# Kernel optimization log

Hardware: AMD Instinct MI355X
Metric: run time of the kernel (lower is better)

The kernel has to match this reference:

```python
import jax, jax.numpy as jnp
import numpy as np

B, N, D, K = 32, 8192, 256, 16
NUM_ITERS = 3
QUALITY_THRESHOLD = 0.3
W_ATTN, W_LEARNED, W_CONF = 0.4, 0.4, 0.2


def _ln(x, g, b, eps=1e-5):
    m = jnp.mean(x, axis=-1, keepdims=True)
    v = jnp.mean((x - m) ** 2, axis=-1, keepdims=True)
    return (x - m) * jax.lax.rsqrt(v + eps) * g + b


def setup_inputs() -> dict:
    key = jax.random.key(0)
    ks = jax.random.split(key, 24)
    s = 0.02
    inp = {
        'inputs': jax.random.normal(ks[0], (B, N, D), dtype=jnp.float32),
        'semantic_confidence': jax.random.uniform(ks[1], (B, K), dtype=jnp.float32),
        'slot_inits': jax.random.normal(ks[2], (K, D), dtype=jnp.float32) * 0.02,
        'ln_in_g': jnp.ones((D,), jnp.float32),
        'ln_in_b': jnp.zeros((D,), jnp.float32),
        'Wq': jax.random.normal(ks[3], (D, D), jnp.float32) * s,
        'Wk': jax.random.normal(ks[4], (D, D), jnp.float32) * s,
        'Wv': jax.random.normal(ks[5], (D, D), jnp.float32) * s,
        'gru_wih': jax.random.normal(ks[6], (3 * D, D), jnp.float32) * s,
        'gru_whh': jax.random.normal(ks[7], (3 * D, D), jnp.float32) * s,
        'gru_bih': jnp.zeros((3 * D,), jnp.float32),
        'gru_bhh': jnp.zeros((3 * D,), jnp.float32),
        'mlp_ln_g': jnp.ones((D,), jnp.float32),
        'mlp_ln_b': jnp.zeros((D,), jnp.float32),
        'mlp_w1': jax.random.normal(ks[8], (2 * D, D), jnp.float32) * s,
        'mlp_b1': jnp.zeros((2 * D,), jnp.float32),
        'mlp_w2': jax.random.normal(ks[9], (D, 2 * D), jnp.float32) * s,
        'mlp_b2': jnp.zeros((D,), jnp.float32),
        'sel_w1': jax.random.normal(ks[10], (D // 2, D), jnp.float32) * s,
        'sel_b1': jnp.zeros((D // 2,), jnp.float32),
        'sel_w2': jax.random.normal(ks[11], (1, D // 2), jnp.float32) * s,
        'sel_b2': jnp.zeros((1,), jnp.float32),
        'qn_w1': jax.random.normal(ks[12], (D // 4, D), jnp.float32) * s,
        'qn_b1': jnp.zeros((D // 4,), jnp.float32),
        'qn_w2': jax.random.normal(ks[13], (1, D // 4), jnp.float32) * s,
        'qn_b2': jnp.zeros((1,), jnp.float32),
    }
    return inp


def _forward(inputs, semantic_confidence, slot_inits, ln_in_g, ln_in_b, Wq, Wk, Wv,
             gru_wih, gru_whh, gru_bih, gru_bhh, mlp_ln_g, mlp_ln_b,
             mlp_w1, mlp_b1, mlp_w2, mlp_b2, sel_w1, sel_b1, sel_w2, sel_b2,
             qn_w1, qn_b1, qn_w2, qn_b2):
    b, n, d = inputs.shape
    kk = slot_inits.shape[0]
    scale = d ** -0.5
    x = _ln(inputs, ln_in_g, ln_in_b)                     # [B,N,D]
    k = x @ Wk.T                                          # [B,N,D] (constant across iters)
    v = x @ Wv.T                                          # [B,N,D]
    slots = jnp.broadcast_to(slot_inits[None], (b, kk, d))
    attn = None
    for _ in range(NUM_ITERS):
        q = slots @ Wq.T                                  # [B,K,D]
        logits = jnp.einsum('bkd,bnd->bkn', q, k) * scale
        attn = jax.nn.softmax(logits, axis=1)             # competition over slots
        updates = jnp.einsum('bkn,bnd->bkd', attn, v)
        # GRUCell: h' = (1-z)*n_g + z*h
        gi = updates @ gru_wih.T + gru_bih                # [B,K,3D]
        gh = slots @ gru_whh.T + gru_bhh
        i_r, i_z, i_n = jnp.split(gi, 3, axis=-1)
        h_r, h_z, h_n = jnp.split(gh, 3, axis=-1)
        r = jax.nn.sigmoid(i_r + h_r)
        z = jax.nn.sigmoid(i_z + h_z)
        n_g = jnp.tanh(i_n + r * h_n)
        slots = (1.0 - z) * n_g + z * slots
        # residual MLP
        h = _ln(slots, mlp_ln_g, mlp_ln_b)
        h = jax.nn.relu(h @ mlp_w1.T + mlp_b1) @ mlp_w2.T + mlp_b2
        slots = slots + h
    final_attn = attn                                     # [B,K,N]
    winners = jnp.argmax(final_attn, axis=1)              # [B,N]
    onehot = (winners[:, None, :] == jnp.arange(kk)[None, :, None]).astype(final_attn.dtype)
    winning_attn = jnp.sum(final_attn * onehot, axis=-1)  # [B,K]
    total_attn = jnp.sum(final_attn, axis=-1)
    attn_quality = winning_attn / (total_attn + 1e-8)
    # learned quality
    lq = jax.nn.relu(slots @ qn_w1.T + qn_b1)
    learned_quality = jax.nn.sigmoid((lq @ qn_w2.T + qn_b2)[..., 0])  # [B,K]
    quality = W_ATTN * attn_quality + W_LEARNED * learned_quality
    quality = quality * W_CONF + semantic_confidence * (1.0 - W_CONF)
    # adaptive selection (eval path: sigmoid threshold)
    sh = jax.nn.relu(slots @ sel_w1.T + sel_b1)
    sel_logits = (sh @ sel_w2.T + sel_b2)[..., 0]         # [B,K]
    sel_mask = (jax.nn.sigmoid(sel_logits) > 0.5).astype(slots.dtype)
    sel_mask = sel_mask * (quality > QUALITY_THRESHOLD).astype(slots.dtype)
    attn_weights = jnp.transpose(final_attn, (0, 2, 1))   # [B,N,K]
    return slots, sel_mask, quality, attn_weights


def reference(inputs, semantic_confidence, slot_inits, ln_in_g, ln_in_b, Wq, Wk, Wv,
              gru_wih, gru_whh, gru_bih, gru_bhh, mlp_ln_g, mlp_ln_b,
              mlp_w1, mlp_b1, mlp_w2, mlp_b2, sel_w1, sel_b1, sel_w2, sel_b2,
              qn_w1, qn_b1, qn_w2, qn_b2):
    return _forward(inputs, semantic_confidence, slot_inits, ln_in_g, ln_in_b, Wq, Wk, Wv,
                    gru_wih, gru_whh, gru_bih, gru_bhh, mlp_ln_g, mlp_ln_b,
                    mlp_w1, mlp_b1, mlp_w2, mlp_b2, sel_w1, sel_b1, sel_w2, sel_b2,
                    qn_w1, qn_b1, qn_w2, qn_b2)
```

## Files before the change

### kernel.cpp

```cpp
#include <hip/hip_runtime.h>

#define BB 32
#define NN 8192
#define DD 256
#define KK 16

typedef __bf16  bf16x8 __attribute__((ext_vector_type(8)));
typedef float   f32x4  __attribute__((ext_vector_type(4)));
typedef unsigned short us8 __attribute__((ext_vector_type(8)));

__device__ __forceinline__ unsigned short f2bf(float f) {
  unsigned u = __builtin_bit_cast(unsigned, f);
  u += 0x7fffu + ((u >> 16) & 1u);
  return (unsigned short)(u >> 16);
}
__device__ __forceinline__ float bf2f(unsigned short h) {
  unsigned u = ((unsigned)h) << 16;
  return __builtin_bit_cast(float, u);
}
__device__ __forceinline__ float sigm(float x) { return 1.f / (1.f + __expf(-x)); }
__device__ __forceinline__ float tanh_fast(float x) { return 1.f - 2.f / (__expf(2.f * x) + 1.f); }

__device__ __forceinline__ void gl2lds16(const void* g, void* l) {
  __builtin_amdgcn_global_load_lds((const __attribute__((address_space(1))) unsigned int*)g,
                                   (__attribute__((address_space(3))) unsigned int*)l, 16, 0, 0);
}

__global__ __launch_bounds__(256) void k_init(const float* __restrict__ Wk, const float* __restrict__ Wv,
                                              const float* __restrict__ sinit,
                                              unsigned short* __restrict__ Wkvb, float* __restrict__ slots) {
  int idx = blockIdx.x * 256 + threadIdx.x;
  int row = idx >> 8, col = idx & 255;
  float w = (row < 256) ? Wk[row * 256 + col] : Wv[(row - 256) * 256 + col];
  Wkvb[idx] = f2bf(w);
  slots[idx] = sinit[(row & 15) * 256 + col];
}

__global__ __launch_bounds__(256) void k_proj(const float* __restrict__ X, const float* __restrict__ lng,
                                              const float* __restrict__ lnb,
                                              const unsigned short* __restrict__ Wkvb,
                                              unsigned short* __restrict__ kv) {
  __shared__ __attribute__((aligned(16))) char bt[2][33280];
  const int wave = threadIdx.x >> 6, lane = threadIdx.x & 63;
  const int c16 = lane & 15, quad = lane >> 4;
  const int row0 = blockIdx.x * 256 + wave * 64;

  bf16x8 af[4][8];
#pragma unroll
  for (int s = 0; s < 4; ++s) {
    const int row = row0 + s * 16 + c16;
    const float* xr = X + (long)row * 256;
    float v[8][8];
    float sum = 0.f, sq = 0.f;
#pragma unroll
    for (int fi = 0; fi < 8; ++fi) {
      const float4 a0 = *(const float4*)(xr + fi * 32 + quad * 8);
      const float4 a1 = *(const float4*)(xr + fi * 32 + quad * 8 + 4);
      v[fi][0] = a0.x; v[fi][1] = a0.y; v[fi][2] = a0.z; v[fi][3] = a0.w;
      v[fi][4] = a1.x; v[fi][5] = a1.y; v[fi][6] = a1.z; v[fi][7] = a1.w;
      sum += a0.x + a0.y + a0.z + a0.w + a1.x + a1.y + a1.z + a1.w;
      sq += a0.x * a0.x + a0.y * a0.y + a0.z * a0.z + a0.w * a0.w +
            a1.x * a1.x + a1.y * a1.y + a1.z * a1.z + a1.w * a1.w;
    }
    sum += __shfl_xor(sum, 16); sum += __shfl_xor(sum, 32);
    sq  += __shfl_xor(sq, 16);  sq  += __shfl_xor(sq, 32);
    const float mean = sum * (1.f / 256.f);
    const float rstd = rsqrtf(sq * (1.f / 256.f) - mean * mean + 1e-5f);
#pragma unroll
    for (int fi = 0; fi < 8; ++fi) {
      const int dbase = fi * 32 + quad * 8;
      const float4 g0 = *(const float4*)(lng + dbase), g1 = *(const float4*)(lng + dbase + 4);
      const float4 b0 = *(const float4*)(lnb + dbase), b1 = *(const float4*)(lnb + dbase + 4);
      us8 t;
      t[0] = f2bf((v[fi][0] - mean) * rstd * g0.x + b0.x);
      t[1] = f2bf((v[fi][1] - mean) * rstd * g0.y + b0.y);
      t[2] = f2bf((v[fi][2] - mean) * rstd * g0.z + b0.z);
      t[3] = f2bf((v[fi][3] - mean) * rstd * g0.w + b0.w);
      t[4] = f2bf((v[fi][4] - mean) * rstd * g1.x + b1.x);
      t[5] = f2bf((v[fi][5] - mean) * rstd * g1.y + b1.y);
      t[6] = f2bf((v[fi][6] - mean) * rstd * g1.z + b1.z);
      t[7] = f2bf((v[fi][7] - mean) * rstd * g1.w + b1.w);
      af[s][fi] = __builtin_bit_cast(bf16x8, t);
    }
  }

  {
    const char* gw = (const char*)Wkvb;
#pragma unroll
    for (int i = 0; i < 8; ++i) {
      const int p = wave * 8 + i;
      gl2lds16(gw + p * 1024 + lane * 16, &bt[0][p * 1040]);
    }
  }
#pragma unroll 1
  for (int c = 0; c < 8; ++c) {
    __syncthreads();
    if (c < 7) {
      const char* gw = (const char*)Wkvb + (c + 1) * 32768;
#pragma unroll
      for (int i = 0; i < 8; ++i) {
        const int p = wave * 8 + i;
        gl2lds16(gw + p * 1024 + lane * 16, &bt[(c + 1) & 1][p * 1040]);
      }
    }
    const char* bb = bt[c & 1];
#pragma unroll 1
    for (int ot = 0; ot < 4; ++ot) {
      const int tl = ot * 16 + c16;
      const char* bp = bb + (tl >> 1) * 1040 + (tl & 1) * 512 + quad * 16;
      f32x4 acc[4];
#pragma unroll
      for (int s = 0; s < 4; ++s) { acc[s][0] = 0.f; acc[s][1] = 0.f; acc[s][2] = 0.f; acc[s][3] = 0.f; }
#pragma unroll
      for (int fi = 0; fi < 8; ++fi) {
        const bf16x8 bfrag = *(const bf16x8*)(bp + fi * 64);
#pragma unroll
        for (int s = 0; s < 4; ++s)
          acc[s] = __builtin_amdgcn_mfma_f32_16x16x32_bf16(af[s][fi], bfrag, acc[s], 0, 0, 0);
      }
      const int col = c * 64 + ot * 16 + c16;
#pragma unroll
      for (int s = 0; s < 4; ++s) {
#pragma unroll
        for (int r = 0; r < 4; ++r) {
          kv[(long)(row0 + s * 16 + quad * 4 + r) * 512 + col] = f2bf(acc[s][r]);
        }
      }
    }
  }
}

__global__ __launch_bounds__(256) void k_qproj(const float* __restrict__ slots, const float* __restrict__ Wq,
                                               unsigned short* __restrict__ qb) {
  __shared__ float srow[256];
  const int row = blockIdx.x, t = threadIdx.x;
  srow[t] = slots[row * 256 + t];
  __syncthreads();
  float acc = 0.f;
  const float4* wr = (const float4*)(Wq + t * 256);
#pragma unroll 8
  for (int i = 0; i < 64; ++i) {
    float4 w = wr[i];
    float4 s = *(const float4*)(srow + i * 4);
    acc += w.x * s.x + w.y * s.y + w.z * s.z + w.w * s.w;
  }
  qb[row * 256 + t] = f2bf(acc);
}

__device__ __forceinline__ void stage_chunk64(const char* gk, char* buf, int wave, int lane) {
#pragma unroll
  for (int i = 0; i < 16; ++i) {
    const int p = wave * 16 + i;
    const int tp = p & 31;
    const int vh = (p >> 5) * 512;
    gl2lds16(gk + (2 * tp + (lane >> 5)) * 1024 + vh + (lane & 31) * 16, buf + p * 1040);
  }
}

template <bool FINAL>
__global__ __launch_bounds__(256) void k_attn(const unsigned short* __restrict__ kv,
                                              const unsigned short* __restrict__ qb,
                                              float* __restrict__ updates, float* __restrict__ aw,
                                              float* __restrict__ winning, float* __restrict__ total) {
  __shared__ __attribute__((aligned(16))) char sbuf[2][66560];
  __shared__ float lds_attn[4][16][16];
  const int wave = threadIdx.x >> 6, lane = threadIdx.x & 63;
  const int c16 = lane & 15, quad = lane >> 4;
  const int b = blockIdx.x >> 3, slab = blockIdx.x & 7;

  bf16x8 qa[8];
  const unsigned short* qrow = qb + (b * 16 + c16) * 256 + quad * 8;
#pragma unroll
  for (int fi = 0; fi < 8; ++fi) qa[fi] = *(const bf16x8*)(qrow + fi * 32);

  float acc[16][4];
#pragma unroll
  for (int s = 0; s < 16; ++s) { acc[s][0] = 0.f; acc[s][1] = 0.f; acc[s][2] = 0.f; acc[s][3] = 0.f; }

  const char* gk0 = (const char*)kv + ((long)b * 8192 + (long)slab * 1024) * 1024;

  stage_chunk64(gk0, sbuf[0], wave, lane);

#pragma unroll 1
  for (int ch = 0; ch < 16; ++ch) {
    __syncthreads();
    if (ch < 15) stage_chunk64(gk0 + (ch + 1) * 65536, sbuf[(ch + 1) & 1], wave, lane);
    const char* bb = sbuf[ch & 1];

    const int tl = wave * 16 + c16;
    const char* kp = bb + (tl >> 1) * 1040 + (tl & 1) * 512 + quad * 16;
    f32x4 c = {0.f, 0.f, 0.f, 0.f};
#pragma unroll
    for (int fi = 0; fi < 8; ++fi) {
      const bf16x8 bfrag = *(const bf16x8*)(kp + fi * 64);
      c = __builtin_amdgcn_mfma_f32_16x16x32_bf16(qa[fi], bfrag, c, 0, 0, 0);
    }
    float l[4];
#pragma unroll
    for (int r = 0; r < 4; ++r) l[r] = c[r] * 0.0625f;
    float m = l[0]; int mi = quad * 4;
#pragma unroll
    for (int r = 1; r < 4; ++r) { if (l[r] > m) { m = l[r]; mi = quad * 4 + r; } }
#pragma unroll
    for (int off = 16; off < 64; off <<= 1) {
      float om = __shfl_xor(m, off); int oi = __shfl_xor(mi, off);
      if (om > m || (om == m && oi < mi)) { m = om; mi = oi; }
    }
    float e[4], ssum = 0.f;
#pragma unroll
    for (int r = 0; r < 4; ++r) { e[r] = __expf(l[r] - m); ssum += e[r]; }
    ssum += __shfl_xor(ssum, 16); ssum += __shfl_xor(ssum, 32);
    const float inv = 1.f / ssum;
    float a[4];
#pragma unroll
    for (int r = 0; r < 4; ++r) a[r] = e[r] * inv;

    if (FINAL) {
      const int tg = slab * 1024 + ch * 64 + wave * 16 + c16;
      *(float4*)(aw + (long)(b * 8192 + tg) * 16 + quad * 4) = make_float4(a[0], a[1], a[2], a[3]);
      float ts[4] = {a[0], a[1], a[2], a[3]};
#pragma unroll
      for (int off = 1; off < 16; off <<= 1) {
#pragma unroll
        for (int r = 0; r < 4; ++r) ts[r] += __shfl_xor(ts[r], off);
      }
      if (c16 == 0) {
#pragma unroll
        for (int r = 0; r < 4; ++r) atomicAdd(&total[b * 16 + quad * 4 + r], ts[r]);
      }
      if (quad == 0) atomicAdd(&winning[b * 16 + mi], inv);
    }

    *(float4*)&lds_attn[wave][c16][quad * 4] = make_float4(a[0], a[1], a[2], a[3]);

#pragma unroll 4
    for (int nn = 0; nn < 16; ++nn) {
      const int n = wave * 16 + nn;
      const char* vp = bb + (32 + (n >> 1)) * 1040 + (n & 1) * 512 + lane * 8;
      const ushort4 vv = *(const ushort4*)vp;
      const float v0 = bf2f(vv.x), v1 = bf2f(vv.y), v2 = bf2f(vv.z), v3 = bf2f(vv.w);
      const float4 a0 = *(const float4*)&lds_attn[wave][nn][0];
      const float4 a1 = *(const float4*)&lds_attn[wave][nn][4];
      const float4 a2 = *(const float4*)&lds_attn[wave][nn][8];
      const float4 a3 = *(const float4*)&lds_attn[wave][nn][12];
      const float as[16] = {a0.x, a0.y, a0.z, a0.w, a1.x, a1.y, a1.z, a1.w,
                            a2.x, a2.y, a2.z, a2.w, a3.x, a3.y, a3.z, a3.w};
#pragma unroll
      for (int s = 0; s < 16; ++s) {
        acc[s][0] = fmaf(as[s], v0, acc[s][0]);
        acc[s][1] = fmaf(as[s], v1, acc[s][1]);
        acc[s][2] = fmaf(as[s], v2, acc[s][2]);
        acc[s][3] = fmaf(as[s], v3, acc[s][3]);
      }
    }
  }

  __syncthreads();
  float* part = (float*)sbuf;
#pragma unroll
  for (int s = 0; s < 16; ++s)
    *(float4*)&part[(wave * 16 + s) * 256 + lane * 4] =
        make_float4(acc[s][0], acc[s][1], acc[s][2], acc[s][3]);
  __syncthreads();
  float* ub = updates + b * (KK * DD);
#pragma unroll
  for (int i = 0; i < 16; ++i) {
    const int idx = i * 256 + threadIdx.x;
    atomicAdd(&ub[idx], part[idx] + part[4096 + idx] + part[8192 + idx] + part[12288 + idx]);
  }
}

__global__ __launch_bounds__(256) void k_slotup(const float* __restrict__ updates, float* __restrict__ slots,
                                                const float* __restrict__ wih, const float* __restrict__ whh,
                                                const float* __restrict__ bih, const float* __restrict__ bhh,
                                                const float* __restrict__ mlng, const float* __restrict__ mlnb,
                                                const float* __restrict__ w1, const float* __restrict__ b1,
                                                const float* __restrict__ w2, const float* __restrict__ b2) {
  __shared__ float su[4][256];
  __shared__ float ss[4][256];
  __shared__ float sn[4][256];
  __shared__ float h1s[4][512];
  __shared__ float mv[8];
  const int t = threadIdx.x;
  const int r0 = blockIdx.x * 4;
#pragma unroll
  for (int r = 0; r < 4; ++r) {
    su[r][t] = updates[(r0 + r) * 256 + t];
    ss[r][t] = slots[(r0 + r) * 256 + t];
  }
  __syncthreads();
  float giv[3][4], ghv[3][4];
#pragma unroll 1
  for (int p = 0; p < 3; ++p) {
    const int o = p * 256 + t;
    float ai[4], ah[4];
    const float bi = bih[o], bh = bhh[o];
#pragma unroll
    for (int r = 0; r < 4; ++r) { ai[r] = bi; ah[r] = bh; }
    const float4* wi = (const float4*)(wih + o * 256);
    const float4* wh = (const float4*)(whh + o * 256);
#pragma unroll 4
    for (int i = 0; i < 64; ++i) {
      const float4 a = wi[i], hh = wh[i];
#pragma unroll
      for (int r = 0; r < 4; ++r) {
        const float4 u = *(const float4*)&su[r][i * 4];
        const float4 s = *(const float4*)&ss[r][i * 4];
        ai[r] += a.x * u.x + a.y * u.y + a.z * u.z + a.w * u.w;
        ah[r] += hh.x * s.x + hh.y * s.y + hh.z * s.z + hh.w * s.w;
      }
    }
#pragma unroll
    for (int r = 0; r < 4; ++r) { giv[p][r] = ai[r]; ghv[p][r] = ah[r]; }
  }
#pragma unroll
  for (int r = 0; r < 4; ++r) {
    const float rg = sigm(giv[0][r] + ghv[0][r]);
    const float z = sigm(giv[1][r] + ghv[1][r]);
    const float ng = tanh_fast(giv[2][r] + rg * ghv[2][r]);
    sn[r][t] = (1.f - z) * ng + z * ss[r][t];
  }
  __syncthreads();
  const int wv = t >> 6, ln = t & 63;
  {
    const float4 x = *(const float4*)&sn[wv][ln * 4];
    float s = x.x + x.y + x.z + x.w;
    float q = x.x * x.x + x.y * x.y + x.z * x.z + x.w * x.w;
#pragma unroll
    for (int off = 1; off < 64; off <<= 1) { s += __shfl_xor(s, off); q += __shfl_xor(q, off); }
    if (ln == 0) {
      const float mean = s * (1.f / 256.f);
      mv[wv * 2] = mean;
      mv[wv * 2 + 1] = rsqrtf(q * (1.f / 256.f) - mean * mean + 1e-5f);
    }
  }
  __syncthreads();
  const float gt = mlng[t], btv = mlnb[t];
#pragma unroll
  for (int r = 0; r < 4; ++r) ss[r][t] = (sn[r][t] - mv[r * 2]) * mv[r * 2 + 1] * gt + btv;
  __syncthreads();
#pragma unroll 1
  for (int p = 0; p < 2; ++p) {
    const int o = p * 256 + t;
    float a1v[4];
    const float bb1 = b1[o];
#pragma unroll
    for (int r = 0; r < 4; ++r) a1v[r] = bb1;
    const float4* wr = (const float4*)(w1 + o * 256);
#pragma unroll 4
    for (int i = 0; i < 64; ++i) {
      const float4 w = wr[i];
#pragma unroll
      for (int r = 0; r < 4; ++r) {
        const float4 hv = *(const float4*)&ss[r][i * 4];
        a1v[r] += w.x * hv.x + w.y * hv.y + w.z * hv.z + w.w * hv.w;
      }
    }
#pragma unroll
    for (int r = 0; r < 4; ++r) h1s[r][o] = fmaxf(a1v[r], 0.f);
  }
  __syncthreads();
  float a2[4];
  const float bb2 = b2[t];
#pragma unroll
  for (int r = 0; r < 4; ++r) a2[r] = bb2;
  const float4* w2r = (const float4*)(w2 + t * 512);
#pragma unroll 4
  for (int i = 0; i < 128; ++i) {
    const float4 w = w2r[i];
#pragma unroll
    for (int r = 0; r < 4; ++r) {
      const float4 hv = *(const float4*)&h1s[r][i * 4];
      a2[r] += w.x * hv.x + w.y * hv.y + w.z * hv.z + w.w * hv.w;
    }
  }
#pragma unroll
  for (int r = 0; r < 4; ++r) slots[(r0 + r) * 256 + t] = sn[r][t] + a2[r];
}

__global__ __launch_bounds__(256) void k_final(const float* __restrict__ slots, const float* __restrict__ winning,
                                               const float* __restrict__ total, const float* __restrict__ conf,
                                               const float* __restrict__ sw1, const float* __restrict__ sb1,
                                               const float* __restrict__ sw2, const float* __restrict__ sb2,
                                               const float* __restrict__ qw1, const float* __restrict__ qb1,
                                               const float* __restrict__ qw2, const float* __restrict__ qb2,
                                               float* __restrict__ out_slots, float* __restrict__ out_mask,
                                               float* __restrict__ out_quality) {
  __shared__ float srow[256];
  __shared__ float sh[128];
  __shared__ float lq[64];
  const int row = blockIdx.x, t = threadIdx.x;
  srow[t] = slots[row * 256 + t];
  __syncthreads();
  if (t < 128) {
    float acc = sb1[t];
    const float4* wr = (const float4*)(sw1 + t * 256);
#pragma unroll 8
    for (int i = 0; i < 64; ++i) {
      const float4 w = wr[i];
      const float4 s = *(const float4*)(srow + i * 4);
      acc += w.x * s.x + w.y * s.y + w.z * s.z + w.w * s.w;
    }
    sh[t] = fmaxf(acc, 0.f);
  } else if (t < 192) {
    const int o = t - 128;
    float acc = qb1[o];
    const float4* wr = (const float4*)(qw1 + o * 256);
#pragma unroll 8
    for (int i = 0; i < 64; ++i) {
      const float4 w = wr[i];
      const float4 s = *(const float4*)(srow + i * 4);
      acc += w.x * s.x + w.y * s.y + w.z * s.z + w.w * s.w;
    }
    lq[o] = fmaxf(acc, 0.f);
  }
  __syncthreads();
  if (t < 64) {
    float a = sh[t] * sw2[t] + sh[t + 64] * sw2[t + 64];
    float bq = lq[t] * qw2[t];
#pragma unroll
    for (int off = 1; off < 64; off <<= 1) { a += __shfl_xor(a, off); bq += __shfl_xor(bq, off); }
    if (t == 0) {
      const float sel_logit = a + sb2[0];
      const float learned = sigm(bq + qb2[0]);
      const float attq = winning[row] / (total[row] + 1e-8f);
      float qual = 0.4f * attq + 0.4f * learned;
      qual = qual * 0.2f + conf[row] * 0.8f;
      out_quality[row] = qual;
      out_mask[row] = (sel_logit > 0.f && qual > 0.3f) ? 1.f : 0.f;
    }
  }
  out_slots[row * 256 + t] = srow[t];
}

extern "C" void kernel_launch(void* const* d_in, const int* in_sizes, int n_in,
                              void* d_out, int out_size, void* d_ws, size_t ws_size,
                              hipStream_t stream) {
  const float* X = (const float*)d_in[0];
  const float* conf = (const float*)d_in[1];
  const float* sinit = (const float*)d_in[2];
  const float* lng = (const float*)d_in[3];
  const float* lnb = (const float*)d_in[4];
  const float* Wq = (const float*)d_in[5];
  const float* Wk = (const float*)d_in[6];
  const float* Wv = (const float*)d_in[7];
  const float* wih = (const float*)d_in[8];
  const float* whh = (const float*)d_in[9];
  const float* bih = (const float*)d_in[10];
  const float* bhh = (const float*)d_in[11];
  const float* mlng = (const float*)d_in[12];
  const float* mlnb = (const float*)d_in[13];
  const float* w1 = (const float*)d_in[14];
  const float* b1 = (const float*)d_in[15];
  const float* w2 = (const float*)d_in[16];
  const float* b2 = (const float*)d_in[17];
  const float* sw1 = (const float*)d_in[18];
  const float* sb1 = (const float*)d_in[19];
  const float* sw2 = (const float*)d_in[20];
  const float* sb2 = (const float*)d_in[21];
  const float* qw1 = (const float*)d_in[22];
  const float* qb1 = (const float*)d_in[23];
  const float* qw2 = (const float*)d_in[24];
  const float* qb2 = (const float*)d_in[25];

  char* w = (char*)d_ws;
  unsigned short* kv = (unsigned short*)(w);
  unsigned short* Wkvb = (unsigned short*)(w + 268435456);
  unsigned short* qb = (unsigned short*)(w + 268697600);
  float* slots = (float*)(w + 268959744);
  float* updates = (float*)(w + 269484032);
  float* winning = (float*)(w + 270008320);
  float* total = (float*)(w + 270010368);

  float* out_slots = (float*)d_out;
  float* out_mask = out_slots + 131072;
  float* out_quality = out_mask + 512;
  float* aw = out_quality + 512;

  k_init<<<512, 256, 0, stream>>>(Wk, Wv, sinit, Wkvb, slots);
  k_proj<<<1024, 256, 0, stream>>>(X, lng, lnb, Wkvb, kv);
  for (int it = 0; it < 3; ++it) {
    k_qproj<<<512, 256, 0, stream>>>(slots, Wq, qb);
    hipMemsetAsync(updates, 0, 512 * 256 * 4, stream);
    if (it == 2) {
      hipMemsetAsync(winning, 0, 2048, stream);
      hipMemsetAsync(total, 0, 2048, stream);
      k_attn<true><<<256, 256, 0, stream>>>(kv, qb, updates, aw, winning, total);
    } else {
      k_attn<false><<<256, 256, 0, stream>>>(kv, qb, updates, nullptr, nullptr, nullptr);
    }
    k_slotup<<<128, 256, 0, stream>>>(updates, slots, wih, whh, bih, bhh, mlng, mlnb, w1, b1, w2, b2);
  }
  k_final<<<512, 256, 0, stream>>>(slots, winning, total, conf, sw1, sb1, sw2, sb2,
                                   qw1, qb1, qw2, qb2, out_slots, out_mask, out_quality);
}
```

Baseline: 1.079 ms.

## Double attention grid with half-size chunks and load K/V weights directly in projection

The attention kernel now launches 512 blocks, each covering 512 tokens in 32-token chunks. Pairs of waves redundantly compute the same logits and split the value accumulation between them, which halves LDS use and adds parallelism on a GPU with many CUs. The projection kernel drops its LDS double-buffering of the weight matrix and reads B fragments straight from global memory. It also swaps the MFMA operands so each lane can write four contiguous bf16 outputs as one vector store. The costs are redundant logit and softmax work in half of the attention waves, and more global weight traffic in the projection.

```diff
diff --git a/kernel.cpp b/kernel.cpp
--- a/kernel.cpp
+++ b/kernel.cpp
@@ -40,7 +40,6 @@
                                               const float* __restrict__ lnb,
                                               const unsigned short* __restrict__ Wkvb,
                                               unsigned short* __restrict__ kv) {
-  __shared__ __attribute__((aligned(16))) char bt[2][33280];
   const int wave = threadIdx.x >> 6, lane = threadIdx.x & 63;
   const int c16 = lane & 15, quad = lane >> 4;
   const int row0 = blockIdx.x * 256 + wave * 64;
@@ -84,47 +83,29 @@
     }
   }
 
-  {
-    const char* gw = (const char*)Wkvb;
-#pragma unroll
-    for (int i = 0; i < 8; ++i) {
-      const int p = wave * 8 + i;
-      gl2lds16(gw + p * 1024 + lane * 16, &bt[0][p * 1040]);
-    }
-  }
 #pragma unroll 1
   for (int c = 0; c < 8; ++c) {
-    __syncthreads();
-    if (c < 7) {
-      const char* gw = (const char*)Wkvb + (c + 1) * 32768;
-#pragma unroll
-      for (int i = 0; i < 8; ++i) {
-        const int p = wave * 8 + i;
-        gl2lds16(gw + p * 1024 + lane * 16, &bt[(c + 1) & 1][p * 1040]);
-      }
-    }
-    const char* bb = bt[c & 1];
 #pragma unroll 1
     for (int ot = 0; ot < 4; ++ot) {
-      const int tl = ot * 16 + c16;
-      const char* bp = bb + (tl >> 1) * 1040 + (tl & 1) * 512 + quad * 16;
+      const unsigned short* wrow = Wkvb + (c * 64 + ot * 16 + c16) * 256 + quad * 8;
+      bf16x8 bfrag[8];
+#pragma unroll
+      for (int fi = 0; fi < 8; ++fi) bfrag[fi] = *(const bf16x8*)(wrow + fi * 32);
       f32x4 acc[4];
 #pragma unroll
       for (int s = 0; s < 4; ++s) { acc[s][0] = 0.f; acc[s][1] = 0.f; acc[s][2] = 0.f; acc[s][3] = 0.f; }
 #pragma unroll
       for (int fi = 0; fi < 8; ++fi) {
-        const bf16x8 bfrag = *(const bf16x8*)(bp + fi * 64);
 #pragma unroll
         for (int s = 0; s < 4; ++s)
-          acc[s] = __builtin_amdgcn_mfma_f32_16x16x32_bf16(af[s][fi], bfrag, acc[s], 0, 0, 0);
-      }
-      const int col = c * 64 + ot * 16 + c16;
+          acc[s] = __builtin_amdgcn_mfma_f32_16x16x32_bf16(bfrag[fi], af[s][fi], acc[s], 0, 0, 0);
+      }
+      const int colb = c * 64 + ot * 16 + quad * 4;
 #pragma unroll
       for (int s = 0; s < 4; ++s) {
-#pragma unroll
-        for (int r = 0; r < 4; ++r) {
-          kv[(long)(row0 + s * 16 + quad * 4 + r) * 512 + col] = f2bf(acc[s][r]);
-        }
+        ushort4 o;
+        o.x = f2bf(acc[s][0]); o.y = f2bf(acc[s][1]); o.z = f2bf(acc[s][2]); o.w = f2bf(acc[s][3]);
+        *(ushort4*)(kv + (long)(row0 + s * 16 + c16) * 512 + colb) = o;
       }
     }
   }
@@ -147,12 +128,12 @@
   qb[row * 256 + t] = f2bf(acc);
 }
 
-__device__ __forceinline__ void stage_chunk64(const char* gk, char* buf, int wave, int lane) {
-#pragma unroll
-  for (int i = 0; i < 16; ++i) {
-    const int p = wave * 16 + i;
-    const int tp = p & 31;
-    const int vh = (p >> 5) * 512;
+__device__ __forceinline__ void stage_chunk32(const char* gk, char* buf, int wave, int lane) {
+#pragma unroll
+  for (int i = 0; i < 8; ++i) {
+    const int p = wave * 8 + i;
+    const int tp = p & 15;
+    const int vh = (p >> 4) * 512;
     gl2lds16(gk + (2 * tp + (lane >> 5)) * 1024 + vh + (lane & 31) * 16, buf + p * 1040);
   }
 }
@@ -162,11 +143,11 @@
                                               const unsigned short* __restrict__ qb,
                                               float* __restrict__ updates, float* __restrict__ aw,
                                               float* __restrict__ winning, float* __restrict__ total) {
-  __shared__ __attribute__((aligned(16))) char sbuf[2][66560];
+  __shared__ __attribute__((aligned(16))) char sbuf[2][33280];
   __shared__ float lds_attn[4][16][16];
   const int wave = threadIdx.x >> 6, lane = threadIdx.x & 63;
   const int c16 = lane & 15, quad = lane >> 4;
-  const int b = blockIdx.x >> 3, slab = blockIdx.x & 7;
+  const int b = blockIdx.x >> 4, slab = blockIdx.x & 15;
 
   bf16x8 qa[8];
   const unsigned short* qrow = qb + (b * 16 + c16) * 256 + quad * 8;
@@ -177,18 +158,18 @@
 #pragma unroll
   for (int s = 0; s < 16; ++s) { acc[s][0] = 0.f; acc[s][1] = 0.f; acc[s][2] = 0.f; acc[s][3] = 0.f; }
 
-  const char* gk0 = (const char*)kv + ((long)b * 8192 + (long)slab * 1024) * 1024;
-
-  stage_chunk64(gk0, sbuf[0], wave, lane);
+  const char* gk0 = (const char*)kv + ((long)b * 8192 + (long)slab * 512) * 1024;
+
+  stage_chunk32(gk0, sbuf[0], wave, lane);
 
 #pragma unroll 1
   for (int ch = 0; ch < 16; ++ch) {
     __syncthreads();
-    if (ch < 15) stage_chunk64(gk0 + (ch + 1) * 65536, sbuf[(ch + 1) & 1], wave, lane);
+    if (ch < 15) stage_chunk32(gk0 + (ch + 1) * 32768, sbuf[(ch + 1) & 1], wave, lane);
     const char* bb = sbuf[ch & 1];
 
-    const int tl = wave * 16 + c16;
-    const char* kp = bb + (tl >> 1) * 1040 + (tl & 1) * 512 + quad * 16;
+    const int t = (wave & 1) * 16 + c16;
+    const char* kp = bb + (t >> 1) * 1040 + (t & 1) * 512 + quad * 16;
     f32x4 c = {0.f, 0.f, 0.f, 0.f};
 #pragma unroll
     for (int fi = 0; fi < 8; ++fi) {
@@ -215,8 +196,8 @@
 #pragma unroll
     for (int r = 0; r < 4; ++r) a[r] = e[r] * inv;
 
-    if (FINAL) {
-      const int tg = slab * 1024 + ch * 64 + wave * 16 + c16;
+    if (FINAL && wave < 2) {
+      const int tg = slab * 512 + ch * 32 + (wave & 1) * 16 + c16;
       *(float4*)(aw + (long)(b * 8192 + tg) * 16 + quad * 4) = make_float4(a[0], a[1], a[2], a[3]);
       float ts[4] = {a[0], a[1], a[2], a[3]};
 #pragma unroll
@@ -233,16 +214,17 @@
 
     *(float4*)&lds_attn[wave][c16][quad * 4] = make_float4(a[0], a[1], a[2], a[3]);
 
+    const int nb = (wave >> 1) * 8;
 #pragma unroll 4
-    for (int nn = 0; nn < 16; ++nn) {
-      const int n = wave * 16 + nn;
-      const char* vp = bb + (32 + (n >> 1)) * 1040 + (n & 1) * 512 + lane * 8;
+    for (int nn = 0; nn < 8; ++nn) {
+      const int n = (wave & 1) * 16 + nb + nn;
+      const char* vp = bb + (16 + (n >> 1)) * 1040 + (n & 1) * 512 + lane * 8;
       const ushort4 vv = *(const ushort4*)vp;
       const float v0 = bf2f(vv.x), v1 = bf2f(vv.y), v2 = bf2f(vv.z), v3 = bf2f(vv.w);
-      const float4 a0 = *(const float4*)&lds_attn[wave][nn][0];
-      const float4 a1 = *(const float4*)&lds_attn[wave][nn][4];
-      const float4 a2 = *(const float4*)&lds_attn[wave][nn][8];
-      const float4 a3 = *(const float4*)&lds_attn[wave][nn][12];
+      const float4 a0 = *(const float4*)&lds_attn[wave][nb + nn][0];
+      const float4 a1 = *(const float4*)&lds_attn[wave][nb + nn][4];
+      const float4 a2 = *(const float4*)&lds_attn[wave][nb + nn][8];
+      const float4 a3 = *(const float4*)&lds_attn[wave][nb + nn][12];
       const float as[16] = {a0.x, a0.y, a0.z, a0.w, a1.x, a1.y, a1.z, a1.w,
                             a2.x, a2.y, a2.z, a2.w, a3.x, a3.y, a3.z, a3.w};
 #pragma unroll
@@ -485,9 +467,9 @@
     if (it == 2) {
       hipMemsetAsync(winning, 0, 2048, stream);
       hipMemsetAsync(total, 0, 2048, stream);
-      k_attn<true><<<256, 256, 0, stream>>>(kv, qb, updates, aw, winning, total);
+      k_attn<true><<<512, 256, 0, stream>>>(kv, qb, updates, aw, winning, total);
     } else {
-      k_attn<false><<<256, 256, 0, stream>>>(kv, qb, updates, nullptr, nullptr, nullptr);
+      k_attn<false><<<512, 256, 0, stream>>>(kv, qb, updates, nullptr, nullptr, nullptr);
     }
     k_slotup<<<128, 256, 0, stream>>>(updates, slots, wih, whh, bih, bhh, mlng, mlnb, w1, b1, w2, b2);
   }
```

After: 1.147 ms. 1.06x slower.
